# Performance work log

Measured on AMD Instinct MI355X. Metric: run time of the kernel, lower is better.

## Reference

```python
import jax, jax.numpy as jnp
import numpy as np

EPS = 1e-5
SLOPE = 0.2
K = 20
BINS = [1, 2, 4, 8, 16, 32]


def knn(x_t, k):
    # x_t: (B, N, C) -> idx (B, N, k) of nearest neighbors (by L2, incl. self)
    xx = jnp.sum(x_t * x_t, axis=-1)  # (B, N)
    pd = 2.0 * jnp.einsum('bnc,bmc->bnm', x_t, x_t) - xx[:, :, None] - xx[:, None, :]
    _, idx = jax.lax.top_k(pd, k)
    return idx


def edge_features(x_t, idx):
    # x_t: (B, N, C), idx: (B, N, k) -> (B, N, k, 2C) = [nbr - ctr, ctr]
    B = x_t.shape[0]
    nbr = x_t[jnp.arange(B)[:, None, None], idx]          # (B, N, k, C) gather
    ctr = jnp.broadcast_to(x_t[:, :, None, :], nbr.shape)
    return jnp.concatenate([nbr - ctr, ctr], axis=-1)


def batchnorm(h, gamma, beta, axes):
    # training-mode BN: normalize with batch statistics over `axes` (channel last)
    m = jnp.mean(h, axis=axes, keepdims=True)
    v = jnp.var(h, axis=axes, keepdims=True)
    return (h - m) * jax.lax.rsqrt(v + EPS) * gamma + beta


def lrelu(h):
    return jnp.where(h >= 0, h, SLOPE * h)


def edgeconv(x_t, W, g, b):
    # 1x1 conv over edge features + BN + LeakyReLU + max over k neighbors
    e = edge_features(x_t, knn(x_t, K))            # (B, N, k, 2C)
    h = jnp.einsum('bnkc,oc->bnko', e, W)          # per-edge GEMM
    h = lrelu(batchnorm(h, g, b, (0, 1, 2)))
    return jnp.max(h, axis=2)                      # (B, N, Cout)


def setup_inputs() -> dict:
    key = jax.random.key(0)
    ks = jax.random.split(key, 8)
    B, N = 4, 2048
    d = {'x': jax.random.normal(ks[0], (B, 3, N), dtype=jnp.float32)}
    # conv weights (out, in); BN gamma=1, beta=0 as in torch init
    d['W1'] = jax.random.normal(ks[1], (64, 6), dtype=jnp.float32) * 0.1
    d['g1'] = jnp.ones((64,), jnp.float32); d['b1'] = jnp.zeros((64,), jnp.float32)
    d['W2'] = jax.random.normal(ks[2], (64, 128), dtype=jnp.float32) * 0.1
    d['g2'] = jnp.ones((64,), jnp.float32); d['b2'] = jnp.zeros((64,), jnp.float32)
    d['W3'] = jax.random.normal(ks[3], (128, 128), dtype=jnp.float32) * 0.1
    d['g3'] = jnp.ones((128,), jnp.float32); d['b3'] = jnp.zeros((128,), jnp.float32)
    d['W4'] = jax.random.normal(ks[4], (256, 256), dtype=jnp.float32) * 0.1
    d['g4'] = jnp.ones((256,), jnp.float32); d['b4'] = jnp.zeros((256,), jnp.float32)
    d['W5'] = jax.random.normal(ks[5], (1024, 512), dtype=jnp.float32) * 0.05
    d['g5'] = jnp.ones((1024,), jnp.float32); d['b5'] = jnp.zeros((1024,), jnp.float32)
    d['Wf'] = jax.random.normal(ks[6], (256, 1024), dtype=jnp.float32) * 0.03
    d['bfeat'] = jax.random.normal(ks[7], (256,), dtype=jnp.float32) * 0.01
    return d


def reference(x, W1, g1, b1, W2, g2, b2, W3, g3, b3, W4, g4, b4, W5, g5, b5, Wf, bfeat):
    B, _, N = x.shape
    x_t = jnp.transpose(x, (0, 2, 1))              # (B, N, 3)
    x1 = edgeconv(x_t, W1, g1, b1)                 # (B, N, 64)
    x2 = edgeconv(x1, W2, g2, b2)                  # (B, N, 64)
    x3 = edgeconv(x2, W3, g3, b3)                  # (B, N, 128)
    x4 = edgeconv(x3, W4, g4, b4)                  # (B, N, 256)
    xc = jnp.concatenate([x1, x2, x3, x4], axis=-1)  # (B, N, 512)
    h = jnp.einsum('bnc,oc->bno', xc, W5)          # (B, N, 1024)
    h = lrelu(batchnorm(h, g5, b5, (0, 1)))
    F = h.shape[-1]
    feats = []
    for nb in BINS:  # horizontal pyramid pooling over contiguous point chunks
        z = h.reshape(B, nb, N // nb, F)
        feats.append(jnp.max(z, axis=2) + jnp.mean(z, axis=2))
    bins = jnp.concatenate(feats, axis=1)          # (B, 63, F)
    out = jnp.einsum('bsf,of->sbo', bins, Wf) + bfeat  # (63, B, 256)
    return out
```

## Files before the change

kernel.cpp:

```cpp
#include <hip/hip_runtime.h>
#include <hip/hip_bf16.h>
#include <cstdint>
#include <cstddef>

#define B_SZ   4
#define N_PTS  2048
#define KNN    20
#define BN_ROWS (B_SZ * N_PTS)
#define EPSV   1e-5f
#define SLOPEV 0.2f

#define MODE_GD   0
#define MODE_DIST 1

typedef __attribute__((ext_vector_type(8))) short bf16x8;
typedef __attribute__((ext_vector_type(4))) float f32x4;

__global__ void k_transpose(const float* __restrict__ x, float* __restrict__ xt,
                            float* __restrict__ xx)
{
    int i = blockIdx.x * 256 + threadIdx.x;
    if (i >= BN_ROWS) return;
    int b = i >> 11, n = i & 2047;
    float v0 = x[((b * 3 + 0) << 11) + n];
    float v1 = x[((b * 3 + 1) << 11) + n];
    float v2 = x[((b * 3 + 2) << 11) + n];
    xt[i * 3 + 0] = v0; xt[i * 3 + 1] = v1; xt[i * 3 + 2] = v2;
    xx[i] = fmaf(v0, v0, fmaf(v1, v1, v2 * v2));
}

__global__ void k_prepw_all(const float* __restrict__ W1, const float* __restrict__ W2,
                            const float* __restrict__ W3, const float* __restrict__ W4,
                            const float* __restrict__ W5, const float* __restrict__ Wf,
                            float* __restrict__ wc, __hip_bfloat16* __restrict__ w5h,
                            float* __restrict__ wft)
{
    int i = blockIdx.x * 256 + threadIdx.x;
    if (i >= 876928) return;
    if (i >= 614784) {
        int e = i - 614784;
        int o = e >> 10, f = e & 1023;
        wft[f * 256 + o] = Wf[e];
        return;
    }
    if (i >= 90496) {
        int e = i - 90496;
        w5h[e] = __float2bfloat16(W5[e]);
        return;
    }
    const float* W; int O, C, off;
    if      (i < 384)   { W = W1; O = 64;  C = 3;   off = 0; }
    else if (i < 8576)  { W = W2; O = 64;  C = 64;  off = 384; }
    else if (i < 24960) { W = W3; O = 128; C = 64;  off = 8576; }
    else                { W = W4; O = 256; C = 128; off = 24960; }
    int e = i - off, j = e / C, c = e - j * C;
    float v;
    if (j < O) v = W[j * 2 * C + c];
    else { int jo = j - O; v = W[jo * 2 * C + C + c] - W[jo * 2 * C + c]; }
    wc[i] = v;
}

template<int MODE, bool VEC>
__launch_bounds__(256)
__global__ void k_mm128(const float* __restrict__ A, int lda,
                        const float* __restrict__ Bm, int ldb,
                        const float* __restrict__ xx, int b0,
                        float* __restrict__ C1, float* __restrict__ C2,
                        int Nn, int Kd)
{
    constexpr int LDA_ = 132;
    constexpr int LDB_ = (MODE == MODE_DIST) ? 132 : 68;
    constexpr int BR   = (MODE == MODE_DIST) ? 4 : 2;
    constexpr int SMEMF = 32 * LDA_ + 32 * LDB_;
    __shared__ float smem[SMEMF];
    float* As = smem;
    float* Bs = smem + 32 * LDA_;
    float* T  = smem;
    const int tid = threadIdx.x;
    const int tx  = tid & 15;
    const int ty  = tid >> 4;

    int m0, n0;
    if constexpr (MODE == MODE_DIST) {
        int t = blockIdx.x;
        int it, jt;
        if (t < 120) {
            int i = 0;
            for (; i < 15; ++i) { int cnt = 15 - i; if (t < cnt) break; t -= cnt; }
            it = i; jt = i + 1 + t;
        } else {
            it = jt = t - 120;
        }
        m0 = it * 128;
        n0 = jt * 128;
    } else {
        m0 = blockIdx.y * 128;
        n0 = blockIdx.x * 64;
    }

    const float* Ab;
    const float* Bb;
    int ldbe;
    if constexpr (MODE == MODE_DIST) {
        const int b = b0 + blockIdx.z;
        Ab = A + (size_t)b * N_PTS * lda;
        Bb = Ab;
        ldbe = lda;
    } else {
        Ab = A; Bb = Bm; ldbe = ldb;
    }

    constexpr int NJH = (MODE == MODE_DIST) ? 2 : 1;
    float acc[2][NJH][4][4] = {};

    for (int k0 = 0; k0 < Kd; k0 += 32) {
        #pragma unroll
        for (int r = 0; r < 4; ++r) {
            int e = r * 256 + tid, row = e >> 3, kq = e & 7;
            if constexpr (VEC) {
                float4 v = *(const float4*)&Ab[(size_t)(m0 + row) * lda + k0 + kq * 4];
                As[(kq * 4 + 0) * LDA_ + row] = v.x;
                As[(kq * 4 + 1) * LDA_ + row] = v.y;
                As[(kq * 4 + 2) * LDA_ + row] = v.z;
                As[(kq * 4 + 3) * LDA_ + row] = v.w;
            } else {
                #pragma unroll
                for (int j = 0; j < 4; ++j) {
                    int kg = k0 + kq * 4 + j;
                    As[(kq * 4 + j) * LDA_ + row] =
                        (kg < Kd) ? Ab[(size_t)(m0 + row) * lda + kg] : 0.f;
                }
            }
        }
        #pragma unroll
        for (int r = 0; r < BR; ++r) {
            int e = r * 256 + tid, row = e >> 3, kq = e & 7;
            if constexpr (VEC) {
                float4 v = *(const float4*)&Bb[(size_t)(n0 + row) * ldbe + k0 + kq * 4];
                Bs[(kq * 4 + 0) * LDB_ + row] = v.x;
                Bs[(kq * 4 + 1) * LDB_ + row] = v.y;
                Bs[(kq * 4 + 2) * LDB_ + row] = v.z;
                Bs[(kq * 4 + 3) * LDB_ + row] = v.w;
            } else {
                #pragma unroll
                for (int j = 0; j < 4; ++j) {
                    int kg = k0 + kq * 4 + j;
                    Bs[(kq * 4 + j) * LDB_ + row] =
                        (kg < Kd) ? Bb[(size_t)(n0 + row) * ldbe + kg] : 0.f;
                }
            }
        }
        __syncthreads();

        if constexpr (VEC) {
            float4 ca0 = *(const float4*)&As[ty * 4];
            float4 ca1 = *(const float4*)&As[64 + ty * 4];
            float4 cb0 = *(const float4*)&Bs[tx * 4];
            float4 cb1 = {};
            if constexpr (MODE == MODE_DIST) cb1 = *(const float4*)&Bs[64 + tx * 4];
            #pragma unroll
            for (int kk = 0; kk < 32; ++kk) {
                float4 na0, na1, nb0, nb1;
                if (kk < 31) {
                    na0 = *(const float4*)&As[(kk + 1) * LDA_ + ty * 4];
                    na1 = *(const float4*)&As[(kk + 1) * LDA_ + 64 + ty * 4];
                    nb0 = *(const float4*)&Bs[(kk + 1) * LDB_ + tx * 4];
                    if constexpr (MODE == MODE_DIST)
                        nb1 = *(const float4*)&Bs[(kk + 1) * LDB_ + 64 + tx * 4];
                }
                float av[2][4] = {{ca0.x,ca0.y,ca0.z,ca0.w},{ca1.x,ca1.y,ca1.z,ca1.w}};
                if constexpr (MODE == MODE_DIST) {
                    float bw[2][4] = {{cb0.x,cb0.y,cb0.z,cb0.w},{cb1.x,cb1.y,cb1.z,cb1.w}};
                    #pragma unroll
                    for (int ih = 0; ih < 2; ++ih)
                        #pragma unroll
                        for (int jh = 0; jh < 2; ++jh)
                            #pragma unroll
                            for (int ii = 0; ii < 4; ++ii)
                                #pragma unroll
                                for (int jj = 0; jj < 4; ++jj)
                                    acc[ih][jh][ii][jj] = fmaf(av[ih][ii], bw[jh][jj], acc[ih][jh][ii][jj]);
                } else {
                    float bw[4] = {cb0.x, cb0.y, cb0.z, cb0.w};
                    #pragma unroll
                    for (int ih = 0; ih < 2; ++ih)
                        #pragma unroll
                        for (int ii = 0; ii < 4; ++ii)
                            #pragma unroll
                            for (int jj = 0; jj < 4; ++jj)
                                acc[ih][0][ii][jj] = fmaf(av[ih][ii], bw[jj], acc[ih][0][ii][jj]);
                }
                if (kk < 31) {
                    ca0 = na0; ca1 = na1; cb0 = nb0;
                    if constexpr (MODE == MODE_DIST) cb1 = nb1;
                }
            }
        } else {
            int klen = Kd - k0; if (klen > 32) klen = 32;
            #pragma unroll 8
            for (int kk = 0; kk < klen; ++kk) {
                float4 a0 = *(const float4*)&As[kk * LDA_ + ty * 4];
                float4 a1 = *(const float4*)&As[kk * LDA_ + 64 + ty * 4];
                float av[2][4] = {{a0.x,a0.y,a0.z,a0.w},{a1.x,a1.y,a1.z,a1.w}};
                if constexpr (MODE == MODE_DIST) {
                    float4 b0q = *(const float4*)&Bs[kk * LDB_ + tx * 4];
                    float4 b1q = *(const float4*)&Bs[kk * LDB_ + 64 + tx * 4];
                    float bw[2][4] = {{b0q.x,b0q.y,b0q.z,b0q.w},{b1q.x,b1q.y,b1q.z,b1q.w}};
                    #pragma unroll
                    for (int ih = 0; ih < 2; ++ih)
                        #pragma unroll
                        for (int jh = 0; jh < 2; ++jh)
                            #pragma unroll
                            for (int ii = 0; ii < 4; ++ii)
                                #pragma unroll
                                for (int jj = 0; jj < 4; ++jj)
                                    acc[ih][jh][ii][jj] = fmaf(av[ih][ii], bw[jh][jj], acc[ih][jh][ii][jj]);
                } else {
                    float4 bq = *(const float4*)&Bs[kk * LDB_ + tx * 4];
                    float bw[4] = {bq.x, bq.y, bq.z, bq.w};
                    #pragma unroll
                    for (int ih = 0; ih < 2; ++ih)
                        #pragma unroll
                        for (int ii = 0; ii < 4; ++ii)
                            #pragma unroll
                            for (int jj = 0; jj < 4; ++jj)
                                acc[ih][0][ii][jj] = fmaf(av[ih][ii], bw[jj], acc[ih][0][ii][jj]);
                }
            }
        }
        __syncthreads();
    }

    if constexpr (MODE == MODE_DIST) {
        const float* xxb = xx + (b0 + blockIdx.z) * N_PTS;
        float xj[2][4];
        #pragma unroll
        for (int jh = 0; jh < 2; ++jh) {
            float4 v = *(const float4*)&xxb[n0 + jh * 64 + tx * 4];
            xj[jh][0] = v.x; xj[jh][1] = v.y; xj[jh][2] = v.z; xj[jh][3] = v.w;
        }
        float xiv[2][4];
        #pragma unroll
        for (int ih = 0; ih < 2; ++ih)
            #pragma unroll
            for (int i = 0; i < 4; ++i)
                xiv[ih][i] = xxb[m0 + ih * 64 + ty * 4 + i];
        const bool diag = (m0 == n0);
        const size_t zoff = (size_t)blockIdx.z * N_PTS;

        #pragma unroll
        for (int ih = 0; ih < 2; ++ih)
            #pragma unroll
            for (int i = 0; i < 4; ++i) {
                int gi = m0 + ih * 64 + ty * 4 + i;
                float xi = xiv[ih][i];
                size_t base = (zoff + gi) * N_PTS;
                #pragma unroll
                for (int jh = 0; jh < 2; ++jh) {
                    int gj = n0 + jh * 64 + tx * 4;
                    float4 v;
                    v.x = 2.f * acc[ih][jh][i][0] - xi - xj[jh][0];
                    v.y = 2.f * acc[ih][jh][i][1] - xi - xj[jh][1];
                    v.z = 2.f * acc[ih][jh][i][2] - xi - xj[jh][2];
                    v.w = 2.f * acc[ih][jh][i][3] - xi - xj[jh][3];
                    if (diag) {
                        if (gi == gj + 0) v.x = 0.f;
                        if (gi == gj + 1) v.y = 0.f;
                        if (gi == gj + 2) v.z = 0.f;
                        if (gi == gj + 3) v.w = 0.f;
                    }
                    *(float4*)&C1[base + gj] = v;
                }
            }

        if (!diag) {
            #pragma unroll
            for (int jh = 0; jh < 2; ++jh) {
                #pragma unroll
                for (int c = 0; c < 4; ++c) {
                    float xjc = xj[jh][c];
                    #pragma unroll
                    for (int ih = 0; ih < 2; ++ih) {
                        float4 tv;
                        tv.x = 2.f * acc[ih][jh][0][c] - xjc - xiv[ih][0];
                        tv.y = 2.f * acc[ih][jh][1][c] - xjc - xiv[ih][1];
                        tv.z = 2.f * acc[ih][jh][2][c] - xjc - xiv[ih][2];
                        tv.w = 2.f * acc[ih][jh][3][c] - xjc - xiv[ih][3];
                        *(float4*)&T[(tx * 4 + c) * LDA_ + ih * 64 + ty * 4] = tv;
                    }
                }
                __syncthreads();
                #pragma unroll
                for (int r = 0; r < 8; ++r) {
                    int e = r * 256 + tid;
                    int jr = e >> 5, c4 = e & 31;
                    float4 tv = *(const float4*)&T[jr * LDA_ + c4 * 4];
                    *(float4*)&C1[(zoff + n0 + jh * 64 + jr) * N_PTS + m0 + c4 * 4] = tv;
                }
                __syncthreads();
            }
        }
    } else {
        const int Oo = Nn >> 1;
        #pragma unroll
        for (int ih = 0; ih < 2; ++ih)
            #pragma unroll
            for (int i = 0; i < 4; ++i) {
                int row = m0 + ih * 64 + ty * 4 + i;
                int colg = n0 + tx * 4;
                float4 v = make_float4(acc[ih][0][i][0], acc[ih][0][i][1],
                                       acc[ih][0][i][2], acc[ih][0][i][3]);
                if (colg < Oo) *(float4*)&C1[(size_t)row * Oo + colg] = v;
                else           *(float4*)&C2[(size_t)row * Oo + colg - Oo] = v;
            }
    }
}

__launch_bounds__(256)
__global__ void k_gemm5(const unsigned short* __restrict__ Ah,
                        const unsigned short* __restrict__ Bh,
                        float* __restrict__ Cf,
                        float* __restrict__ ssum, float* __restrict__ ssumsq)
{
    constexpr int LDA = 72;
    __shared__ unsigned short As[128 * LDA];
    __shared__ unsigned short Bs[128 * LDA];
    const int tid  = threadIdx.x;
    const int lane = tid & 63;
    const int w    = tid >> 6;
    const int wr   = w >> 1, wcl = w & 1;
    const int quad = lane >> 4;
    const int l16  = lane & 15;
    const int m0 = blockIdx.y * 128;
    const int n0 = blockIdx.x * 128;

    f32x4 acc[4][4] = {};

    for (int k0 = 0; k0 < 512; k0 += 64) {
        #pragma unroll
        for (int r = 0; r < 4; ++r) {
            int e = r * 256 + tid, row = e >> 3, kq = e & 7;
            *(uint4*)&As[row * LDA + kq * 8] =
                *(const uint4*)&Ah[(size_t)(m0 + row) * 512 + k0 + kq * 8];
        }
        #pragma unroll
        for (int r = 0; r < 4; ++r) {
            int e = r * 256 + tid, row = e >> 3, kq = e & 7;
            *(uint4*)&Bs[row * LDA + kq * 8] =
                *(const uint4*)&Bh[(size_t)(n0 + row) * 512 + k0 + kq * 8];
        }
        __syncthreads();
        #pragma unroll
        for (int kk = 0; kk < 64; kk += 32) {
            bf16x8 af[4], bfr[4];
            #pragma unroll
            for (int i = 0; i < 4; ++i)
                af[i] = *(const bf16x8*)&As[(wr * 64 + i * 16 + l16) * LDA + kk + quad * 8];
            #pragma unroll
            for (int j = 0; j < 4; ++j)
                bfr[j] = *(const bf16x8*)&Bs[(wcl * 64 + j * 16 + l16) * LDA + kk + quad * 8];
            #pragma unroll
            for (int i = 0; i < 4; ++i)
                #pragma unroll
                for (int j = 0; j < 4; ++j)
                    acc[i][j] = __builtin_amdgcn_mfma_f32_16x16x32_bf16(af[i], bfr[j], acc[i][j], 0, 0, 0);
        }
        __syncthreads();
    }

    #pragma unroll
    for (int i = 0; i < 4; ++i) {
        int rbase = m0 + wr * 64 + i * 16 + quad * 4;
        #pragma unroll
        for (int j = 0; j < 4; ++j) {
            int col = n0 + wcl * 64 + j * 16 + l16;
            #pragma unroll
            for (int r = 0; r < 4; ++r)
                Cf[(size_t)(rbase + r) * 1024 + col] = acc[i][j][r];
        }
    }

    float* sredS = (float*)As;
    float* sredQ = (float*)Bs;
    #pragma unroll
    for (int j = 0; j < 4; ++j) {
        float s = 0.f, q = 0.f;
        #pragma unroll
        for (int i = 0; i < 4; ++i)
            #pragma unroll
            for (int r = 0; r < 4; ++r) {
                float v = acc[i][j][r];
                s += v; q = fmaf(v, v, q);
            }
        int coll = wcl * 64 + j * 16 + l16;
        int slot = wr * 4 + quad;
        sredS[coll * 8 + slot] = s;
        sredQ[coll * 8 + slot] = q;
    }
    __syncthreads();
    if (tid < 128) {
        float s = 0.f, q = 0.f;
        #pragma unroll
        for (int t = 0; t < 8; ++t) { s += sredS[tid * 8 + t]; q += sredQ[tid * 8 + t]; }
        ssum  [blockIdx.y * 1024 + n0 + tid] = s;
        ssumsq[blockIdx.y * 1024 + n0 + tid] = q;
    }
}

__launch_bounds__(256)
__global__ void k_select(const float* __restrict__ D2, int* __restrict__ idx_out)
{
    const int lane = threadIdx.x & 63;
    const int w    = threadIdx.x >> 6;
    const int qloc = blockIdx.x * 4 + w;
    const float* row = D2 + (size_t)qloc * N_PTS;

    unsigned key[32];
    #pragma unroll
    for (int c = 0; c < 8; ++c) {
        float4 v = *(const float4*)&row[c * 256 + lane * 4];
        float vv[4] = {v.x, v.y, v.z, v.w};
        #pragma unroll
        for (int r = 0; r < 4; ++r) {
            unsigned u = __float_as_uint(vv[r]);
            key[c * 4 + r] = ((int)u >= 0) ? (u | 0x80000000u) : ~u;
        }
    }

    unsigned lo = 0u, hi = 0xFFFFFFFFu;
    while (lo < hi) {
        unsigned mid = lo + ((hi - lo) >> 1);
        int cnt = 0;
        #pragma unroll
        for (int e = 0; e < 32; ++e)
            cnt += __popcll(__ballot(key[e] > mid));
        if (cnt < KNN) hi = mid; else lo = mid + 1;
    }
    const unsigned T = lo;

    int* outp = idx_out + (size_t)qloc * KNN;
    const unsigned long long ltmask = (lane == 0) ? 0ull : (~0ull >> (64 - lane));
    int base = 0;
    #pragma unroll
    for (int e = 0; e < 32; ++e) {
        bool p = key[e] > T;
        unsigned long long m = __ballot(p);
        if (p) {
            int pos = base + __popcll(m & ltmask);
            outp[pos] = (e >> 2) * 256 + lane * 4 + (e & 3);
        }
        base += __popcll(m);
    }
    #pragma unroll
    for (int e = 0; e < 32; ++e) {
        bool p = key[e] == T;
        unsigned long long m = __ballot(p);
        if (p) {
            int pos = base + __popcll(m & ltmask);
            if (pos < KNN) outp[pos] = (e >> 2) * 256 + lane * 4 + (e & 3);
        }
        base += __popcll(m);
    }
}

template<int O, int NSEQ>
__launch_bounds__(256)
__global__ void k_gather(const float* __restrict__ gtab, const float* __restrict__ dtab,
                         const int* __restrict__ idx,
                         float* __restrict__ hmax, float* __restrict__ hmin,
                         float* __restrict__ ssum, float* __restrict__ ssumsq)
{
    constexpr int NPB = 256 / O;
    const int grp = threadIdx.x / O;
    const int o   = threadIdx.x & (O - 1);
    float accS = 0.f, accS2 = 0.f;
    const int rowsPerBlock = NPB * NSEQ;
    const int batch = blockIdx.x & 3;
    const int chunk = blockIdx.x >> 2;
    const int bbase = batch << 11;
    for (int s = 0; s < NSEQ; ++s) {
        int row = bbase + chunk * rowsPerBlock + s * NPB + grp;
        const int* ip = idx + (size_t)row * KNN;
        float gmax = -INFINITY, gmin = INFINITY, gs = 0.f, gs2 = 0.f;
        for (int k = 0; k < KNN; ++k) {
            int nb = ip[k];
            float v = gtab[(size_t)(bbase + nb) * O + o];
            gmax = fmaxf(gmax, v);
            gmin = fminf(gmin, v);
            gs  += v;
            gs2  = fmaf(v, v, gs2);
        }
        float d = dtab[(size_t)row * O + o];
        hmax[(size_t)row * O + o] = gmax + d;
        hmin[(size_t)row * O + o] = gmin + d;
        accS  += gs + (float)KNN * d;
        accS2 += gs2 + 2.f * d * gs + (float)KNN * d * d;
    }
    int bank = blockIdx.x & 63;
    atomicAdd(&ssum[bank * O + o], accS);
    atomicAdd(&ssumsq[bank * O + o], accS2);
}

template<int O, bool WRITE_XX>
__launch_bounds__(256)
__global__ void k_normalize(const float* __restrict__ hmax, const float* __restrict__ hmin,
                            const float* __restrict__ ssum, const float* __restrict__ ssumsq,
                            const float* __restrict__ gamma, const float* __restrict__ beta,
                            float invM, float* __restrict__ xcs,
                            __hip_bfloat16* __restrict__ xch, float* __restrict__ xx)
{
    const int tid = threadIdx.x;
    const int o   = tid & (O - 1);
    float s = 0.f, s2 = 0.f;
    #pragma unroll 8
    for (int bk = 0; bk < 64; ++bk) { s += ssum[bk * O + o]; s2 += ssumsq[bk * O + o]; }
    float mean = s * invM;
    float var  = fmaf(-mean, mean, s2 * invM);
    float sc   = gamma[o] * rsqrtf(var + EPSV);
    float sh   = beta[o] - mean * sc;

    constexpr int R = 256 / O;
    const int rloc = tid / O;
    __shared__ float part[4];
    const int ngroups = BN_ROWS / R;
    for (int gidx = blockIdx.x; gidx < ngroups; gidx += gridDim.x) {
        int row = gidx * R + rloc;
        size_t i = (size_t)row * O + o;
        float h = (sc >= 0.f) ? hmax[i] : hmin[i];
        float y = fmaf(h, sc, sh);
        y = (y >= 0.f) ? y : SLOPEV * y;
        xcs[(size_t)row * 512 + o] = y;
        xch[(size_t)row * 512 + o] = __float2bfloat16(y);
        if constexpr (WRITE_XX) {
            float p = y * y;
            #pragma unroll
            for (int sft = 32; sft >= 1; sft >>= 1) p += __shfl_xor(p, sft, 64);
            if constexpr (O == 64) {
                if ((tid & 63) == 0) xx[row] = p;
            } else {
                if ((tid & 63) == 0) part[tid >> 6] = p;
                __syncthreads();
                if constexpr (O == 128) {
                    if (tid < 2) xx[gidx * R + tid] = part[2 * tid] + part[2 * tid + 1];
                } else {
                    if (tid == 0) xx[gidx * R] = (part[0] + part[1]) + (part[2] + part[3]);
                }
                __syncthreads();
            }
        }
    }
}

__global__ void k_seg(const float* __restrict__ h,
                      const float* __restrict__ ssum, const float* __restrict__ ssumsq,
                      const float* __restrict__ gamma, const float* __restrict__ beta,
                      float* __restrict__ smax, float* __restrict__ ssumseg)
{
    int f = blockIdx.y * 256 + threadIdx.x;
    float s = 0.f, s2 = 0.f;
    #pragma unroll 8
    for (int bk = 0; bk < 64; ++bk) { s += ssum[bk * 1024 + f]; s2 += ssumsq[bk * 1024 + f]; }
    const float invM = 1.f / (float)BN_ROWS;
    float mean = s * invM;
    float var  = fmaf(-mean, mean, s2 * invM);
    float sc   = gamma[f] * rsqrtf(var + EPSV);
    float sh   = beta[f] - mean * sc;

    int seg = blockIdx.x;
    float mx = -INFINITY, sm = 0.f;
    int n0 = seg * 64;
    for (int i = 0; i < 64; ++i) {
        float v = fmaf(h[(size_t)(n0 + i) * 1024 + f], sc, sh);
        v = (v >= 0.f) ? v : SLOPEV * v;
        mx = fmaxf(mx, v); sm += v;
    }
    smax[(size_t)seg * 1024 + f]    = mx;
    ssumseg[(size_t)seg * 1024 + f] = sm;
}

__launch_bounds__(256)
__global__ void k_final(const float* __restrict__ smax, const float* __restrict__ ssg,
                        const float* __restrict__ Wft, const float* __restrict__ bfeat,
                        float* __restrict__ out)
{
    __shared__ float row[1024];
    __shared__ float part[1024];
    const int tid = threadIdx.x;
    int sb = blockIdx.x;
    int s = sb >> 2, b = sb & 3;
    int nb = (s == 0) ? 1 : (s < 3) ? 2 : (s < 7) ? 4 : (s < 15) ? 8 : (s < 31) ? 16 : 32;
    int idxL = s - (nb - 1);
    int segc = 32 / nb;
    int seg0 = b * 32 + idxL * segc;
    float inv = 1.f / (float)(64 * segc);
    for (int c = tid; c < 1024; c += 256) {
        float mx = -INFINITY, sm = 0.f;
        for (int t = 0; t < segc; ++t) {
            mx = fmaxf(mx, smax[(size_t)(seg0 + t) * 1024 + c]);
            sm += ssg[(size_t)(seg0 + t) * 1024 + c];
        }
        row[c] = mx + sm * inv;
    }
    __syncthreads();

    const int lane = tid & 63;
    const int w    = tid >> 6;
    const float* rw = row + w * 256;
    const float* wp = Wft + (size_t)(w * 256) * 256 + lane * 4;
    float4 a0 = {0,0,0,0}, a1 = {0,0,0,0}, a2 = {0,0,0,0}, a3 = {0,0,0,0};
    for (int f = 0; f < 256; f += 4) {
        float r0 = rw[f + 0], r1 = rw[f + 1], r2 = rw[f + 2], r3 = rw[f + 3];
        float4 w0 = *(const float4*)&wp[(size_t)(f + 0) * 256];
        float4 w1 = *(const float4*)&wp[(size_t)(f + 1) * 256];
        float4 w2 = *(const float4*)&wp[(size_t)(f + 2) * 256];
        float4 w3 = *(const float4*)&wp[(size_t)(f + 3) * 256];
        a0.x = fmaf(r0, w0.x, a0.x); a0.y = fmaf(r0, w0.y, a0.y);
        a0.z = fmaf(r0, w0.z, a0.z); a0.w = fmaf(r0, w0.w, a0.w);
        a1.x = fmaf(r1, w1.x, a1.x); a1.y = fmaf(r1, w1.y, a1.y);
        a1.z = fmaf(r1, w1.z, a1.z); a1.w = fmaf(r1, w1.w, a1.w);
        a2.x = fmaf(r2, w2.x, a2.x); a2.y = fmaf(r2, w2.y, a2.y);
        a2.z = fmaf(r2, w2.z, a2.z); a2.w = fmaf(r2, w2.w, a2.w);
        a3.x = fmaf(r3, w3.x, a3.x); a3.y = fmaf(r3, w3.y, a3.y);
        a3.z = fmaf(r3, w3.z, a3.z); a3.w = fmaf(r3, w3.w, a3.w);
    }
    float4 a;
    a.x = (a0.x + a1.x) + (a2.x + a3.x);
    a.y = (a0.y + a1.y) + (a2.y + a3.y);
    a.z = (a0.z + a1.z) + (a2.z + a3.z);
    a.w = (a0.w + a1.w) + (a2.w + a3.w);
    *(float4*)&part[w * 256 + lane * 4] = a;
    __syncthreads();
    int o = tid;
    float acc = (part[o] + part[256 + o]) + (part[512 + o] + part[768 + o]);
    out[(size_t)sb * 256 + o] = acc + bfeat[o];
}

extern "C" void kernel_launch(void* const* d_in, const int* in_sizes, int n_in,
                              void* d_out, int out_size, void* d_ws, size_t ws_size,
                              hipStream_t stream)
{
    const float* x  = (const float*)d_in[0];
    const float* W1 = (const float*)d_in[1];
    const float* g1 = (const float*)d_in[2];
    const float* b1 = (const float*)d_in[3];
    const float* W2 = (const float*)d_in[4];
    const float* g2 = (const float*)d_in[5];
    const float* b2 = (const float*)d_in[6];
    const float* W3 = (const float*)d_in[7];
    const float* g3 = (const float*)d_in[8];
    const float* b3 = (const float*)d_in[9];
    const float* W4 = (const float*)d_in[10];
    const float* g4 = (const float*)d_in[11];
    const float* b4 = (const float*)d_in[12];
    const float* W5 = (const float*)d_in[13];
    const float* g5 = (const float*)d_in[14];
    const float* b5 = (const float*)d_in[15];
    const float* Wf = (const float*)d_in[16];
    const float* bfeat = (const float*)d_in[17];
    float* out = (float*)d_out;
    float* ws  = (float*)d_ws;

    float* xt1   = ws + 0;
    int*   idx   = (int*)(ws + 24576);
    float* xx    = ws + 188416;
    float* xc    = ws + 196608;
    float* hmax  = ws + 4390912;
    float* hmin  = ws + 6488064;
    float* stats = ws + 8585216;
    float* smax  = ws + 8650752;
    float* ssg   = ws + 8781824;
    float* wc    = ws + 8912896;
    float* big   = ws + 9003520;
    float* gtab  = big;
    float* dtab  = big + 2097152;
    __hip_bfloat16* xch = (__hip_bfloat16*)(ws + 25780736);
    __hip_bfloat16* w5h = (__hip_bfloat16*)(ws + 27877888);
    float* wft   = ws + 28140032;
    float* l5s   = ws + 28402176;
    float* l5q   = ws + 28467712;

    hipMemsetAsync(stats, 0, 65536 * sizeof(float), stream);
    k_transpose<<<32, 256, 0, stream>>>(x, xt1, xx);
    k_prepw_all<<<3426, 256, 0, stream>>>(W1, W2, W3, W4, W5, Wf, wc, w5h, wft);

    const float invMk = 1.f / (float)(BN_ROWS * KNN);

    {
        float* ss = stats + 0;
        k_mm128<MODE_DIST, false><<<dim3(136, 1, 4), 256, 0, stream>>>(xt1, 3, nullptr, 0, xx, 0, big, nullptr, N_PTS, 3);
        k_select<<<2048, 256, 0, stream>>>(big, idx);
        k_mm128<MODE_GD, false><<<dim3(2, 64, 1), 256, 0, stream>>>(xt1, 3, wc, 3, nullptr, 0, gtab, dtab, 128, 3);
        k_gather<64, 8><<<256, 256, 0, stream>>>(gtab, dtab, idx, hmax, hmin, ss, ss + 4096);
        k_normalize<64, true><<<512, 256, 0, stream>>>(hmax, hmin, ss, ss + 4096, g1, b1, invMk, xc + 0, xch + 0, xx);
    }
    {
        float* ss = stats + 8192;
        k_mm128<MODE_DIST, true><<<dim3(136, 1, 4), 256, 0, stream>>>(xc + 0, 512, nullptr, 0, xx, 0, big, nullptr, N_PTS, 64);
        k_select<<<2048, 256, 0, stream>>>(big, idx);
        k_mm128<MODE_GD, true><<<dim3(2, 64, 1), 256, 0, stream>>>(xc + 0, 512, wc + 384, 64, nullptr, 0, gtab, dtab, 128, 64);
        k_gather<64, 8><<<256, 256, 0, stream>>>(gtab, dtab, idx, hmax, hmin, ss, ss + 4096);
        k_normalize<64, true><<<512, 256, 0, stream>>>(hmax, hmin, ss, ss + 4096, g2, b2, invMk, xc + 64, xch + 64, xx);
    }
    {
        float* ss = stats + 16384;
        k_mm128<MODE_DIST, true><<<dim3(136, 1, 4), 256, 0, stream>>>(xc + 64, 512, nullptr, 0, xx, 0, big, nullptr, N_PTS, 64);
        k_select<<<2048, 256, 0, stream>>>(big, idx);
        k_mm128<MODE_GD, true><<<dim3(4, 64, 1), 256, 0, stream>>>(xc + 64, 512, wc + 8576, 64, nullptr, 0, gtab, dtab, 256, 64);
        k_gather<128, 8><<<512, 256, 0, stream>>>(gtab, dtab, idx, hmax, hmin, ss, ss + 8192);
        k_normalize<128, true><<<512, 256, 0, stream>>>(hmax, hmin, ss, ss + 8192, g3, b3, invMk, xc + 128, xch + 128, xx);
    }
    {
        float* ss = stats + 32768;
        k_mm128<MODE_DIST, true><<<dim3(136, 1, 4), 256, 0, stream>>>(xc + 128, 512, nullptr, 0, xx, 0, big, nullptr, N_PTS, 128);
        k_select<<<2048, 256, 0, stream>>>(big, idx);
        k_mm128<MODE_GD, true><<<dim3(8, 64, 1), 256, 0, stream>>>(xc + 128, 512, wc + 24960, 128, nullptr, 0, gtab, dtab, 512, 128);
        k_gather<256, 8><<<1024, 256, 0, stream>>>(gtab, dtab, idx, hmax, hmin, ss, ss + 16384);
        k_normalize<256, false><<<512, 256, 0, stream>>>(hmax, hmin, ss, ss + 16384, g4, b4, invMk, xc + 256, xch + 256, xx);
    }
    {
        k_gemm5<<<dim3(8, 64), 256, 0, stream>>>((const unsigned short*)xch, (const unsigned short*)w5h, big, l5s, l5q);
        k_seg<<<dim3(128, 4), 256, 0, stream>>>(big, l5s, l5q, g5, b5, smax, ssg);
        k_final<<<252, 256, 0, stream>>>(smax, ssg, wft, bfeat, out);
    }
}
```

Measured before the change: 563.7 us.

## Fuse kNN selection and per-point GD GEMM into one launch

After: 544.8 us. 1.03x faster.

```diff
diff --git a/kernel.cpp b/kernel.cpp
--- a/kernel.cpp
+++ b/kernel.cpp
@@ -407,12 +407,133 @@
     }
 }
 
+template<bool VEC>
 __launch_bounds__(256)
-__global__ void k_select(const float* __restrict__ D2, int* __restrict__ idx_out)
-{
+__global__ void k_selgd(const float* __restrict__ D2, int* __restrict__ idx_out,
+                        const float* __restrict__ A, int lda,
+                        const float* __restrict__ Bm, int ldb,
+                        float* __restrict__ C1, float* __restrict__ C2,
+                        int Nn, int Kd, int gdBlocks, int gdsh)
+{
+    constexpr int LDA_ = 132;
+    constexpr int LDB_ = 68;
+    __shared__ float smem[32 * LDA_ + 32 * LDB_];
+
+    if ((int)blockIdx.x < gdBlocks) {
+        float* As = smem;
+        float* Bs = smem + 32 * LDA_;
+        const int tid = threadIdx.x;
+        const int tx  = tid & 15;
+        const int ty  = tid >> 4;
+        const int gdx = Nn >> 6;
+        const int bx  = blockIdx.x & (gdx - 1);
+        const int by  = blockIdx.x >> gdsh;
+        const int m0 = by * 128;
+        const int n0 = bx * 64;
+
+        float acc[2][4][4] = {};
+
+        for (int k0 = 0; k0 < Kd; k0 += 32) {
+            #pragma unroll
+            for (int r = 0; r < 4; ++r) {
+                int e = r * 256 + tid, row = e >> 3, kq = e & 7;
+                if constexpr (VEC) {
+                    float4 v = *(const float4*)&A[(size_t)(m0 + row) * lda + k0 + kq * 4];
+                    As[(kq * 4 + 0) * LDA_ + row] = v.x;
+                    As[(kq * 4 + 1) * LDA_ + row] = v.y;
+                    As[(kq * 4 + 2) * LDA_ + row] = v.z;
+                    As[(kq * 4 + 3) * LDA_ + row] = v.w;
+                } else {
+                    #pragma unroll
+                    for (int j = 0; j < 4; ++j) {
+                        int kg = k0 + kq * 4 + j;
+                        As[(kq * 4 + j) * LDA_ + row] =
+                            (kg < Kd) ? A[(size_t)(m0 + row) * lda + kg] : 0.f;
+                    }
+                }
+            }
+            #pragma unroll
+            for (int r = 0; r < 2; ++r) {
+                int e = r * 256 + tid, row = e >> 3, kq = e & 7;
+                if constexpr (VEC) {
+                    float4 v = *(const float4*)&Bm[(size_t)(n0 + row) * ldb + k0 + kq * 4];
+                    Bs[(kq * 4 + 0) * LDB_ + row] = v.x;
+                    Bs[(kq * 4 + 1) * LDB_ + row] = v.y;
+                    Bs[(kq * 4 + 2) * LDB_ + row] = v.z;
+                    Bs[(kq * 4 + 3) * LDB_ + row] = v.w;
+                } else {
+                    #pragma unroll
+                    for (int j = 0; j < 4; ++j) {
+                        int kg = k0 + kq * 4 + j;
+                        Bs[(kq * 4 + j) * LDB_ + row] =
+                            (kg < Kd) ? Bm[(size_t)(n0 + row) * ldb + kg] : 0.f;
+                    }
+                }
+            }
+            __syncthreads();
+
+            if constexpr (VEC) {
+                float4 ca0 = *(const float4*)&As[ty * 4];
+                float4 ca1 = *(const float4*)&As[64 + ty * 4];
+                float4 cb0 = *(const float4*)&Bs[tx * 4];
+                #pragma unroll
+                for (int kk = 0; kk < 32; ++kk) {
+                    float4 na0, na1, nb0;
+                    if (kk < 31) {
+                        na0 = *(const float4*)&As[(kk + 1) * LDA_ + ty * 4];
+                        na1 = *(const float4*)&As[(kk + 1) * LDA_ + 64 + ty * 4];
+                        nb0 = *(const float4*)&Bs[(kk + 1) * LDB_ + tx * 4];
+                    }
+                    float av[2][4] = {{ca0.x,ca0.y,ca0.z,ca0.w},{ca1.x,ca1.y,ca1.z,ca1.w}};
+                    float bw[4] = {cb0.x, cb0.y, cb0.z, cb0.w};
+                    #pragma unroll
+                    for (int ih = 0; ih < 2; ++ih)
+                        #pragma unroll
+                        for (int ii = 0; ii < 4; ++ii)
+                            #pragma unroll
+                            for (int jj = 0; jj < 4; ++jj)
+                                acc[ih][ii][jj] = fmaf(av[ih][ii], bw[jj], acc[ih][ii][jj]);
+                    if (kk < 31) { ca0 = na0; ca1 = na1; cb0 = nb0; }
+                }
+            } else {
+                int klen = Kd - k0; if (klen > 32) klen = 32;
+                #pragma unroll 8
+                for (int kk = 0; kk < klen; ++kk) {
+                    float4 a0 = *(const float4*)&As[kk * LDA_ + ty * 4];
+                    float4 a1 = *(const float4*)&As[kk * LDA_ + 64 + ty * 4];
+                    float4 bq = *(const float4*)&Bs[kk * LDB_ + tx * 4];
+                    float av[2][4] = {{a0.x,a0.y,a0.z,a0.w},{a1.x,a1.y,a1.z,a1.w}};
+                    float bw[4] = {bq.x, bq.y, bq.z, bq.w};
+                    #pragma unroll
+                    for (int ih = 0; ih < 2; ++ih)
+                        #pragma unroll
+                        for (int ii = 0; ii < 4; ++ii)
+                            #pragma unroll
+                            for (int jj = 0; jj < 4; ++jj)
+                                acc[ih][ii][jj] = fmaf(av[ih][ii], bw[jj], acc[ih][ii][jj]);
+                }
+            }
+            __syncthreads();
+        }
+
+        const int Oo = Nn >> 1;
+        #pragma unroll
+        for (int ih = 0; ih < 2; ++ih)
+            #pragma unroll
+            for (int i = 0; i < 4; ++i) {
+                int row = m0 + ih * 64 + ty * 4 + i;
+                int colg = n0 + tx * 4;
+                float4 v = make_float4(acc[ih][i][0], acc[ih][i][1],
+                                       acc[ih][i][2], acc[ih][i][3]);
+                if (colg < Oo) *(float4*)&C1[(size_t)row * Oo + colg] = v;
+                else           *(float4*)&C2[(size_t)row * Oo + colg - Oo] = v;
+            }
+        return;
+    }
+
     const int lane = threadIdx.x & 63;
     const int w    = threadIdx.x >> 6;
-    const int qloc = blockIdx.x * 4 + w;
+    const int qloc = ((int)blockIdx.x - gdBlocks) * 4 + w;
     const float* row = D2 + (size_t)qloc * N_PTS;
 
     unsigned key[32];
@@ -671,13 +792,13 @@
     float* ssg   = ws + 8781824;
     float* wc    = ws + 8912896;
     float* big   = ws + 9003520;
-    float* gtab  = big;
-    float* dtab  = big + 2097152;
     __hip_bfloat16* xch = (__hip_bfloat16*)(ws + 25780736);
     __hip_bfloat16* w5h = (__hip_bfloat16*)(ws + 27877888);
     float* wft   = ws + 28140032;
     float* l5s   = ws + 28402176;
     float* l5q   = ws + 28467712;
+    float* gtab  = ws + 28533248;
+    float* dtab  = ws + 30630400;
 
     hipMemsetAsync(stats, 0, 65536 * sizeof(float), stream);
     k_transpose<<<32, 256, 0, stream>>>(x, xt1, xx);
@@ -688,32 +809,28 @@
     {
         float* ss = stats + 0;
         k_mm128<MODE_DIST, false><<<dim3(136, 1, 4), 256, 0, stream>>>(xt1, 3, nullptr, 0, xx, 0, big, nullptr, N_PTS, 3);
-        k_select<<<2048, 256, 0, stream>>>(big, idx);
-        k_mm128<MODE_GD, false><<<dim3(2, 64, 1), 256, 0, stream>>>(xt1, 3, wc, 3, nullptr, 0, gtab, dtab, 128, 3);
+        k_selgd<false><<<128 + 2048, 256, 0, stream>>>(big, idx, xt1, 3, wc, 3, gtab, dtab, 128, 3, 128, 1);
         k_gather<64, 8><<<256, 256, 0, stream>>>(gtab, dtab, idx, hmax, hmin, ss, ss + 4096);
         k_normalize<64, true><<<512, 256, 0, stream>>>(hmax, hmin, ss, ss + 4096, g1, b1, invMk, xc + 0, xch + 0, xx);
     }
     {
         float* ss = stats + 8192;
         k_mm128<MODE_DIST, true><<<dim3(136, 1, 4), 256, 0, stream>>>(xc + 0, 512, nullptr, 0, xx, 0, big, nullptr, N_PTS, 64);
-        k_select<<<2048, 256, 0, stream>>>(big, idx);
-        k_mm128<MODE_GD, true><<<dim3(2, 64, 1), 256, 0, stream>>>(xc + 0, 512, wc + 384, 64, nullptr, 0, gtab, dtab, 128, 64);
+        k_selgd<true><<<128 + 2048, 256, 0, stream>>>(big, idx, xc + 0, 512, wc + 384, 64, gtab, dtab, 128, 64, 128, 1);
         k_gather<64, 8><<<256, 256, 0, stream>>>(gtab, dtab, idx, hmax, hmin, ss, ss + 4096);
         k_normalize<64, true><<<512, 256, 0, stream>>>(hmax, hmin, ss, ss + 4096, g2, b2, invMk, xc + 64, xch + 64, xx);
     }
     {
         float* ss = stats + 16384;
         k_mm128<MODE_DIST, true><<<dim3(136, 1, 4), 256, 0, stream>>>(xc + 64, 512, nullptr, 0, xx, 0, big, nullptr, N_PTS, 64);
-        k_select<<<2048, 256, 0, stream>>>(big, idx);
-        k_mm128<MODE_GD, true><<<dim3(4, 64, 1), 256, 0, stream>>>(xc + 64, 512, wc + 8576, 64, nullptr, 0, gtab, dtab, 256, 64);
+        k_selgd<true><<<256 + 2048, 256, 0, stream>>>(big, idx, xc + 64, 512, wc + 8576, 64, gtab, dtab, 256, 64, 256, 2);
         k_gather<128, 8><<<512, 256, 0, stream>>>(gtab, dtab, idx, hmax, hmin, ss, ss + 8192);
         k_normalize<128, true><<<512, 256, 0, stream>>>(hmax, hmin, ss, ss + 8192, g3, b3, invMk, xc + 128, xch + 128, xx);
     }
     {
         float* ss = stats + 32768;
         k_mm128<MODE_DIST, true><<<dim3(136, 1, 4), 256, 0, stream>>>(xc + 128, 512, nullptr, 0, xx, 0, big, nullptr, N_PTS, 128);
-        k_select<<<2048, 256, 0, stream>>>(big, idx);
-        k_mm128<MODE_GD, true><<<dim3(8, 64, 1), 256, 0, stream>>>(xc + 128, 512, wc + 24960, 128, nullptr, 0, gtab, dtab, 512, 128);
+        k_selgd<true><<<512 + 2048, 256, 0, stream>>>(big, idx, xc + 128, 512, wc + 24960, 128, gtab, dtab, 512, 128, 512, 3);
         k_gather<256, 8><<<1024, 256, 0, stream>>>(gtab, dtab, idx, hmax, hmin, ss, ss + 16384);
         k_normalize<256, false><<<512, 256, 0, stream>>>(hmax, hmin, ss, ss + 16384, g4, b4, invMk, xc + 256, xch + 256, xx);
     }
```
